# Optimization experiments

Hardware: AMD Instinct MI355X
Metric: run time of the kernel (lower is better)

The kernel has to match this reference:

```python
import jax, jax.numpy as jnp
import numpy as np

H = 8  # num_heads
EPS = 1e-5


def _lin_params(key, din, dout, scale=0.02):
    kw, _ = jax.random.split(key)
    W = jax.random.normal(kw, (din, dout), jnp.float32) * scale
    b = jnp.zeros((dout,), jnp.float32)
    return W, b


def _edge_attention(x_src, x_dst, ei, ea, Wq, bq, Wk, bk, Wv, bv, We, be, Wo, bo, n_dst):
    out_c = Wq.shape[1]
    D = out_c // H
    scale = D ** -0.5
    q = (x_dst @ Wq + bq).reshape(-1, H, D)
    k = (x_src @ Wk + bk).reshape(-1, H, D)
    v = (x_src @ Wv + bv).reshape(-1, H, D)
    e = (ea @ We + be).reshape(-1, H, D)
    src, dst = ei[0], ei[1]
    ke = k[src] + e                                # [E,H,D]
    ve = v[src] + e                                # [E,H,D]
    s = jnp.einsum('ehd,ehd->eh', q[dst], ke) * scale  # [E,H]
    # segment (per-destination) softmax, numerically stable
    m = jax.ops.segment_max(s, dst, num_segments=n_dst)
    ex = jnp.exp(s - m[dst])
    den = jax.ops.segment_sum(ex, dst, num_segments=n_dst)
    a = ex / den[dst]                              # [E,H]  (dropout = identity in eval)
    agg = jax.ops.segment_sum(a[..., None] * ve, dst, num_segments=n_dst)  # [N_dst,H,D]
    return agg.reshape(n_dst, out_c) @ Wo + bo


def _layernorm(x, g, b):
    mu = jnp.mean(x, axis=-1, keepdims=True)
    var = jnp.mean((x - mu) ** 2, axis=-1, keepdims=True)
    return (x - mu) * jax.lax.rsqrt(var + EPS) * g + b


def setup_inputs() -> dict:
    key = jax.random.key(0)
    ks = jax.random.split(key, 32)
    N_pc, N_gr, E_pp, E_pg = 50000, 8000, 400000, 100000
    din, dout, de = 128, 128, 64
    inp = {}
    inp['x_pc'] = jax.random.normal(ks[0], (N_pc, din), jnp.float32)
    inp['x_gr'] = jax.random.normal(ks[1], (N_gr, din), jnp.float32)
    inp['ea_pp'] = jax.random.normal(ks[2], (E_pp, de), jnp.float32)
    inp['ea_pg'] = jax.random.normal(ks[3], (E_pg, de), jnp.float32)
    inp['ei_pp'] = jax.random.randint(ks[4], (2, E_pp), 0, N_pc, jnp.int32)
    src_pg = jax.random.randint(ks[5], (E_pg,), 0, N_pc, jnp.int32)
    dst_pg = jax.random.randint(ks[6], (E_pg,), 0, N_gr, jnp.int32)
    inp['ei_pg'] = jnp.stack([src_pg, dst_pg])
    i = 7
    for et in ('pp', 'pg'):
        for nm, d_in in (('Wq', din), ('Wk', din), ('Wv', din), ('We', de), ('Wo', dout)):
            W, b = _lin_params(ks[i], d_in, dout); i += 1
            inp[f'{nm}_{et}'] = W
            inp[f'b{nm[1].lower()}_{et}'] = b
    for nt, d_in in (('pc', din), ('gr', din)):
        W, b = _lin_params(ks[i], d_in, dout); i += 1
        inp[f'Wnp_{nt}'] = W
        inp[f'bnp_{nt}'] = b
        inp[f'g_{nt}'] = jnp.ones((dout,), jnp.float32)
        inp[f'bln_{nt}'] = jnp.zeros((dout,), jnp.float32)
    return inp


def reference(x_pc, x_gr, ea_pp, ea_pg, ei_pp, ei_pg,
              Wq_pp, bq_pp, Wk_pp, bk_pp, Wv_pp, bv_pp, We_pp, be_pp, Wo_pp, bo_pp,
              Wq_pg, bq_pg, Wk_pg, bk_pg, Wv_pg, bv_pg, We_pg, be_pg, Wo_pg, bo_pg,
              Wnp_pc, bnp_pc, Wnp_gr, bnp_gr, g_pc, bln_pc, g_gr, bln_gr):
    N_pc, N_gr = x_pc.shape[0], x_gr.shape[0]
    out_pc = x_pc @ Wnp_pc + bnp_pc
    out_gr = x_gr @ Wnp_gr + bnp_gr
    out_pc = out_pc + _edge_attention(x_pc, x_pc, ei_pp, ea_pp,
                                      Wq_pp, bq_pp, Wk_pp, bk_pp, Wv_pp, bv_pp,
                                      We_pp, be_pp, Wo_pp, bo_pp, N_pc)
    out_gr = out_gr + _edge_attention(x_pc, x_gr, ei_pg, ea_pg,
                                      Wq_pg, bq_pg, Wk_pg, bk_pg, Wv_pg, bv_pg,
                                      We_pg, be_pg, Wo_pg, bo_pg, N_gr)
    out_pc = _layernorm(out_pc, g_pc, bln_pc)
    out_gr = _layernorm(out_gr, g_gr, bln_gr)
    return out_pc, out_gr
```

## Files before the change

kernel.cpp:

```cpp
#include <hip/hip_runtime.h>
#include <hip/hip_bf16.h>
#include <stdint.h>

typedef short short8 __attribute__((ext_vector_type(8)));
typedef float f32x4 __attribute__((ext_vector_type(4)));

__device__ __forceinline__ unsigned short f2bf(float x) {
    unsigned u = __float_as_uint(x);
    u += 0x7fffu + ((u >> 16) & 1u);
    return (unsigned short)(u >> 16);
}
__device__ __forceinline__ float bf2f(unsigned short u) {
    return __uint_as_float(((unsigned)u) << 16);
}

struct WDesc { const float* src; unsigned short* dst; int K, ldd, koff; };
struct WPack { WDesc w[12]; };

__global__ __launch_bounds__(256) void prep_weights(WPack p) {
    WDesc d = p.w[blockIdx.x];
    int total = d.K * 128;
    for (int i = threadIdx.x; i < total; i += 256) {
        int n = i / d.K, k = i - n * d.K;
        d.dst[(size_t)n * d.ldd + d.koff + k] = f2bf(d.src[(size_t)k * 128 + n]);
    }
}

struct NodeOut { const unsigned short* Wt; const float* bias; unsigned short* out; int ldc, coloff; };
struct NodePack { NodeOut d[5]; };

template <int NOUT>
__global__ __launch_bounds__(256) void gemm_node(const float* __restrict__ A, int M, NodePack dp) {
    constexpr int K = 128, LDA = 136, LDB = 72, TLD = 136;
    __shared__ __align__(16) unsigned short As[64 * LDA];
    __shared__ __align__(16) unsigned short Bs[128 * LDB];

    const int tid = threadIdx.x;
    const int rbase = blockIdx.x * 64;

    for (int slot = tid; slot < 64 * 16; slot += 256) {
        int row = slot >> 4, kg = slot & 15;
        int gr = rbase + row;
        short8 s8 = {0, 0, 0, 0, 0, 0, 0, 0};
        if (gr < M) {
            const float* a = A + (size_t)gr * K + kg * 8;
            float4 f0 = *reinterpret_cast<const float4*>(a);
            float4 f1 = *reinterpret_cast<const float4*>(a + 4);
            s8[0] = (short)f2bf(f0.x); s8[1] = (short)f2bf(f0.y);
            s8[2] = (short)f2bf(f0.z); s8[3] = (short)f2bf(f0.w);
            s8[4] = (short)f2bf(f1.x); s8[5] = (short)f2bf(f1.y);
            s8[6] = (short)f2bf(f1.z); s8[7] = (short)f2bf(f1.w);
        }
        *reinterpret_cast<short8*>(&As[row * LDA + kg * 8]) = s8;
    }

    const int lane = tid & 63, w = tid >> 6;
    const int rb = (w >> 1) * 32, cb = (w & 1) * 64;
    const int qd = lane >> 4, l16 = lane & 15;

    for (int o = 0; o < NOUT; ++o) {
        NodeOut d = dp.d[o];
        f32x4 acc[2][4];
#pragma unroll
        for (int rt = 0; rt < 2; ++rt)
#pragma unroll
            for (int ct = 0; ct < 4; ++ct) { f32x4 z = {0.f,0.f,0.f,0.f}; acc[rt][ct] = z; }

        for (int kc = 0; kc < K; kc += 64) {
            __syncthreads();
            for (int slot = tid; slot < 128 * 8; slot += 256) {
                int n = slot >> 3, kg = slot & 7;
                *reinterpret_cast<short8*>(&Bs[n * LDB + kg * 8]) =
                    *reinterpret_cast<const short8*>(d.Wt + (size_t)n * K + kc + kg * 8);
            }
            __syncthreads();
#pragma unroll
            for (int ks = 0; ks < 64; ks += 32) {
                short8 af[2], bfr[4];
#pragma unroll
                for (int rt = 0; rt < 2; ++rt)
                    af[rt] = *reinterpret_cast<const short8*>(
                        &As[(rb + rt * 16 + l16) * LDA + kc + ks + qd * 8]);
#pragma unroll
                for (int ct = 0; ct < 4; ++ct)
                    bfr[ct] = *reinterpret_cast<const short8*>(
                        &Bs[(cb + ct * 16 + l16) * LDB + ks + qd * 8]);
#pragma unroll
                for (int rt = 0; rt < 2; ++rt)
#pragma unroll
                    for (int ct = 0; ct < 4; ++ct)
                        acc[rt][ct] = __builtin_amdgcn_mfma_f32_16x16x32_bf16(
                            af[rt], bfr[ct], acc[rt][ct], 0, 0, 0);
            }
        }

        __syncthreads();
        unsigned short* tile = Bs;
#pragma unroll
        for (int ct = 0; ct < 4; ++ct) {
            int col = cb + ct * 16 + l16;
            float bv = d.bias[col];
#pragma unroll
            for (int rt = 0; rt < 2; ++rt)
#pragma unroll
                for (int r = 0; r < 4; ++r)
                    tile[(rb + rt * 16 + qd * 4 + r) * TLD + col] = f2bf(acc[rt][ct][r] + bv);
        }
        __syncthreads();
#pragma unroll
        for (int rep = 0; rep < 4; ++rep) {
            int lrow = (tid >> 4) + rep * 16, seg = tid & 15;
            int gr = rbase + lrow;
            if (gr < M)
                *reinterpret_cast<short8*>(&d.out[(size_t)gr * d.ldc + d.coloff + seg * 8]) =
                    *reinterpret_cast<const short8*>(&tile[lrow * TLD + seg * 8]);
        }
    }
}

struct EdgePack {
    const float* A; const unsigned short* Wt; const float* bias;
    const int* pos; unsigned short* out; int M;
};

__global__ __launch_bounds__(256) void gemm_edge(EdgePack p0, EdgePack p1, int B0) {
    constexpr int K = 64, LDA = 72, LDB = 72, TLD = 136;
    __shared__ __align__(16) unsigned short As[64 * LDA];
    __shared__ __align__(16) unsigned short Bs[128 * LDB];

    EdgePack p; int blk;
    if (blockIdx.x < B0) { p = p0; blk = blockIdx.x; } else { p = p1; blk = blockIdx.x - B0; }

    const int tid = threadIdx.x;
    const int rbase = blk * 64;

    for (int slot = tid; slot < 64 * 8; slot += 256) {
        int row = slot >> 3, kg = slot & 7;
        int gr = rbase + row;
        short8 s8 = {0, 0, 0, 0, 0, 0, 0, 0};
        if (gr < p.M) {
            const float* a = p.A + (size_t)gr * K + kg * 8;
            float4 f0 = *reinterpret_cast<const float4*>(a);
            float4 f1 = *reinterpret_cast<const float4*>(a + 4);
            s8[0] = (short)f2bf(f0.x); s8[1] = (short)f2bf(f0.y);
            s8[2] = (short)f2bf(f0.z); s8[3] = (short)f2bf(f0.w);
            s8[4] = (short)f2bf(f1.x); s8[5] = (short)f2bf(f1.y);
            s8[6] = (short)f2bf(f1.z); s8[7] = (short)f2bf(f1.w);
        }
        *reinterpret_cast<short8*>(&As[row * LDA + kg * 8]) = s8;
    }
    for (int slot = tid; slot < 128 * 8; slot += 256) {
        int n = slot >> 3, kg = slot & 7;
        *reinterpret_cast<short8*>(&Bs[n * LDB + kg * 8]) =
            *reinterpret_cast<const short8*>(p.Wt + (size_t)n * K + kg * 8);
    }
    __syncthreads();

    const int lane = tid & 63, w = tid >> 6;
    const int rb = (w >> 1) * 32, cb = (w & 1) * 64;
    const int qd = lane >> 4, l16 = lane & 15;

    f32x4 acc[2][4];
#pragma unroll
    for (int rt = 0; rt < 2; ++rt)
#pragma unroll
        for (int ct = 0; ct < 4; ++ct) { f32x4 z = {0.f,0.f,0.f,0.f}; acc[rt][ct] = z; }

#pragma unroll
    for (int ks = 0; ks < 64; ks += 32) {
        short8 af[2], bfr[4];
#pragma unroll
        for (int rt = 0; rt < 2; ++rt)
            af[rt] = *reinterpret_cast<const short8*>(&As[(rb + rt * 16 + l16) * LDA + ks + qd * 8]);
#pragma unroll
        for (int ct = 0; ct < 4; ++ct)
            bfr[ct] = *reinterpret_cast<const short8*>(&Bs[(cb + ct * 16 + l16) * LDB + ks + qd * 8]);
#pragma unroll
        for (int rt = 0; rt < 2; ++rt)
#pragma unroll
            for (int ct = 0; ct < 4; ++ct)
                acc[rt][ct] = __builtin_amdgcn_mfma_f32_16x16x32_bf16(
                    af[rt], bfr[ct], acc[rt][ct], 0, 0, 0);
    }

    __syncthreads();
    unsigned short* tile = Bs;
#pragma unroll
    for (int ct = 0; ct < 4; ++ct) {
        int col = cb + ct * 16 + l16;
        float bv = p.bias[col];
#pragma unroll
        for (int rt = 0; rt < 2; ++rt)
#pragma unroll
            for (int r = 0; r < 4; ++r)
                tile[(rb + rt * 16 + qd * 4 + r) * TLD + col] = f2bf(acc[rt][ct][r] + bv);
    }
    __syncthreads();
#pragma unroll
    for (int rep = 0; rep < 4; ++rep) {
        int lrow = (tid >> 4) + rep * 16, seg = tid & 15;
        int gr = rbase + lrow;
        if (gr < p.M) {
            int dp = p.pos[gr];
            *reinterpret_cast<short8*>(&p.out[(size_t)dp * 128 + seg * 8]) =
                *reinterpret_cast<const short8*>(&tile[lrow * TLD + seg * 8]);
        }
    }
}

struct OutPack {
    const unsigned short* Aagg; const float* Ax;
    const unsigned short* Wt;
    const float *bo, *bnp, *g, *bln; float* out; int M;
};

__global__ __launch_bounds__(256) void gemm_out_ln(OutPack p0, OutPack p1, int B0) {
    constexpr int K = 256, LDA = 264, LDB = 72, FTLD = 132;
    __shared__ __align__(16) char smemA[64 * LDA * 2];
    __shared__ __align__(16) unsigned short Bs[128 * LDB];
    unsigned short* As = (unsigned short*)smemA;

    OutPack p; int blk;
    if (blockIdx.x < B0) { p = p0; blk = blockIdx.x; } else { p = p1; blk = blockIdx.x - B0; }

    const int tid = threadIdx.x;
    const int rbase = blk * 64;

    for (int slot = tid; slot < 64 * 32; slot += 256) {
        int row = slot >> 5, kg = slot & 31;
        int gr = rbase + row;
        short8 s8 = {0, 0, 0, 0, 0, 0, 0, 0};
        if (gr < p.M) {
            if (kg < 16) {
                s8 = *reinterpret_cast<const short8*>(p.Aagg + (size_t)gr * 128 + kg * 8);
            } else {
                const float* a = p.Ax + (size_t)gr * 128 + (kg - 16) * 8;
                float4 f0 = *reinterpret_cast<const float4*>(a);
                float4 f1 = *reinterpret_cast<const float4*>(a + 4);
                s8[0] = (short)f2bf(f0.x); s8[1] = (short)f2bf(f0.y);
                s8[2] = (short)f2bf(f0.z); s8[3] = (short)f2bf(f0.w);
                s8[4] = (short)f2bf(f1.x); s8[5] = (short)f2bf(f1.y);
                s8[6] = (short)f2bf(f1.z); s8[7] = (short)f2bf(f1.w);
            }
        }
        *reinterpret_cast<short8*>(&As[row * LDA + kg * 8]) = s8;
    }

    const int lane = tid & 63, w = tid >> 6;
    const int rb = (w >> 1) * 32, cb = (w & 1) * 64;
    const int qd = lane >> 4, l16 = lane & 15;

    f32x4 acc[2][4];
#pragma unroll
    for (int rt = 0; rt < 2; ++rt)
#pragma unroll
        for (int ct = 0; ct < 4; ++ct) { f32x4 z = {0.f,0.f,0.f,0.f}; acc[rt][ct] = z; }

    for (int kc = 0; kc < K; kc += 64) {
        __syncthreads();
        for (int slot = tid; slot < 128 * 8; slot += 256) {
            int n = slot >> 3, kg = slot & 7;
            *reinterpret_cast<short8*>(&Bs[n * LDB + kg * 8]) =
                *reinterpret_cast<const short8*>(p.Wt + (size_t)n * K + kc + kg * 8);
        }
        __syncthreads();
#pragma unroll
        for (int ks = 0; ks < 64; ks += 32) {
            short8 af[2], bfr[4];
#pragma unroll
            for (int rt = 0; rt < 2; ++rt)
                af[rt] = *reinterpret_cast<const short8*>(
                    &As[(rb + rt * 16 + l16) * LDA + kc + ks + qd * 8]);
#pragma unroll
            for (int ct = 0; ct < 4; ++ct)
                bfr[ct] = *reinterpret_cast<const short8*>(
                    &Bs[(cb + ct * 16 + l16) * LDB + ks + qd * 8]);
#pragma unroll
            for (int rt = 0; rt < 2; ++rt)
#pragma unroll
                for (int ct = 0; ct < 4; ++ct)
                    acc[rt][ct] = __builtin_amdgcn_mfma_f32_16x16x32_bf16(
                        af[rt], bfr[ct], acc[rt][ct], 0, 0, 0);
        }
    }

    __syncthreads();
    float* ftile = (float*)smemA;
#pragma unroll
    for (int ct = 0; ct < 4; ++ct) {
        int col = cb + ct * 16 + l16;
        float bv = p.bo[col] + p.bnp[col];
#pragma unroll
        for (int rt = 0; rt < 2; ++rt)
#pragma unroll
            for (int r = 0; r < 4; ++r)
                ftile[(rb + rt * 16 + qd * 4 + r) * FTLD + col] = acc[rt][ct][r] + bv;
    }
    __syncthreads();

    int r = tid >> 2, q4 = tid & 3;
    const float* rowp = &ftile[r * FTLD + q4 * 32];
    float s = 0.f, sq = 0.f;
#pragma unroll
    for (int j = 0; j < 8; ++j) {
        float4 v = *reinterpret_cast<const float4*>(rowp + j * 4);
        s += v.x + v.y + v.z + v.w;
        sq += v.x * v.x + v.y * v.y + v.z * v.z + v.w * v.w;
    }
    s += __shfl_xor(s, 1, 64);  s += __shfl_xor(s, 2, 64);
    sq += __shfl_xor(sq, 1, 64); sq += __shfl_xor(sq, 2, 64);
    float mu = s * (1.f / 128.f);
    float var = sq * (1.f / 128.f) - mu * mu;
    float rs = rsqrtf(var + 1e-5f);
    int gr = rbase + r;
    if (gr < p.M) {
#pragma unroll
        for (int j = 0; j < 8; ++j) {
            float4 v = *reinterpret_cast<const float4*>(rowp + j * 4);
            int c = q4 * 32 + j * 4;
            float4 gg = *reinterpret_cast<const float4*>(p.g + c);
            float4 bb = *reinterpret_cast<const float4*>(p.bln + c);
            float4 o;
            o.x = (v.x - mu) * rs * gg.x + bb.x;
            o.y = (v.y - mu) * rs * gg.y + bb.y;
            o.z = (v.z - mu) * rs * gg.z + bb.z;
            o.w = (v.w - mu) * rs * gg.w + bb.w;
            *reinterpret_cast<float4*>(&p.out[(size_t)gr * 128 + c]) = o;
        }
    }
}

__global__ __launch_bounds__(256) void count_both(const int* __restrict__ d0, int E0, int* c0,
                                                  const int* __restrict__ d1, int E1, int* c1) {
    int t = blockIdx.x * 256 + threadIdx.x;
    if (t < E0) atomicAdd(&c0[d0[t]], 1);
    else if (t < E0 + E1) atomicAdd(&c1[d1[t - E0]], 1);
}

__global__ __launch_bounds__(1024) void scan_partial(const int* c0, int N0, int* rp0, int* bs0, int B0,
                                                     const int* c1, int N1, int* rp1, int* bs1) {
    __shared__ int wsum[16];
    const int* c; int* rp; int* bs; int N; int blk;
    if ((int)blockIdx.x < B0) { c = c0; rp = rp0; bs = bs0; N = N0; blk = blockIdx.x; }
    else { c = c1; rp = rp1; bs = bs1; N = N1; blk = blockIdx.x - B0; }
    int tid = threadIdx.x, lane = tid & 63, w = tid >> 6;
    int i = blk * 1024 + tid;
    int v = (i < N) ? c[i] : 0;
    int s = v;
#pragma unroll
    for (int off = 1; off < 64; off <<= 1) {
        int t = __shfl_up(s, off, 64);
        if (lane >= off) s += t;
    }
    if (lane == 63) wsum[w] = s;
    __syncthreads();
    if (w == 0 && lane < 16) {
        int ws = wsum[lane];
#pragma unroll
        for (int off = 1; off < 16; off <<= 1) {
            int t = __shfl_up(ws, off, 64);
            if (lane >= off) ws += t;
        }
        wsum[lane] = ws;
    }
    __syncthreads();
    int wexcl = (w == 0) ? 0 : wsum[w - 1];
    if (i < N) rp[i] = wexcl + s - v;
    if (tid == 0) bs[blk] = wsum[15];
}

__global__ __launch_bounds__(128) void scan_mid(const int* bs0, int* off0, int B0, int* rpN0,
                                                const int* bs1, int* off1, int B1, int* rpN1) {
    int w = threadIdx.x >> 6, lane = threadIdx.x & 63;
    const int* bs = w ? bs1 : bs0;
    int* off = w ? off1 : off0;
    int B = w ? B1 : B0;
    int* rpN = w ? rpN1 : rpN0;
    int v = (lane < B) ? bs[lane] : 0;
    int s = v;
#pragma unroll
    for (int o = 1; o < 64; o <<= 1) {
        int t = __shfl_up(s, o, 64);
        if (lane >= o) s += t;
    }
    if (lane < B) off[lane] = s - v;
    int total = __shfl(s, B - 1, 64);
    if (lane == 0) *rpN = total;
}

__global__ __launch_bounds__(1024) void scan_add(int* rp0, int* cur0, const int* off0, int N0, int B0,
                                                 int* rp1, int* cur1, const int* off1, int N1) {
    int* rp; int* cur; const int* off; int N; int blk;
    if ((int)blockIdx.x < B0) { rp = rp0; cur = cur0; off = off0; N = N0; blk = blockIdx.x; }
    else { rp = rp1; cur = cur1; off = off1; N = N1; blk = blockIdx.x - B0; }
    int i = blk * 1024 + threadIdx.x;
    if (i < N) {
        int vv = rp[i] + off[blk];
        rp[i] = vv;
        cur[i] = vv;
    }
}

__global__ __launch_bounds__(256) void scatter_both(
    const int* __restrict__ s0, const int* __restrict__ d0, int E0, int* cur0, int* pos0, int* srcs0,
    const int* __restrict__ s1, const int* __restrict__ d1, int E1, int* cur1, int* pos1, int* srcs1) {
    int t = blockIdx.x * 256 + threadIdx.x;
    if (t < E0) {
        int p = atomicAdd(&cur0[d0[t]], 1);
        pos0[t] = p;
        srcs0[p] = s0[t];
    } else if (t < E0 + E1) {
        int tt = t - E0;
        int p = atomicAdd(&cur1[d1[tt]], 1);
        pos1[tt] = p;
        srcs1[p] = s1[tt];
    }
}

struct AttnPack {
    const unsigned short *q, *kv, *e;
    const int *srcs, *row_ptr;
    unsigned short* agg; int N;
};

__global__ __launch_bounds__(256) void attn_gather(AttnPack a0, AttnPack a1, int B0) {
    AttnPack a; int blk;
    if ((int)blockIdx.x < B0) { a = a0; blk = blockIdx.x; } else { a = a1; blk = blockIdx.x - B0; }
    int wl = (blk * 256 + threadIdx.x) >> 6;
    int dst = wl >> 1;
    if (dst >= a.N) return;
    int lane = threadIdx.x & 63;
    int col = ((wl & 1) << 6) + lane;

    float qf = bf2f(a.q[(size_t)dst * 128 + col]);
    int beg = a.row_ptr[dst], end = a.row_ptr[dst + 1];
    float den = 0.f, acc = 0.f;

    float kfC = 0.f, vfC = 0.f, efC = 0.f;
    int sB = 0;
    if (beg < end) {
        int s0 = a.srcs[beg];
        kfC = bf2f(a.kv[(size_t)s0 * 256 + col]);
        vfC = bf2f(a.kv[(size_t)s0 * 256 + 128 + col]);
        efC = bf2f(a.e[(size_t)beg * 128 + col]);
        if (beg + 1 < end) sB = a.srcs[beg + 1];
    }
    for (int i = beg; i < end; ++i) {
        float kfN = 0.f, vfN = 0.f, efN = 0.f;
        int sC = 0;
        if (i + 1 < end) {
            kfN = bf2f(a.kv[(size_t)sB * 256 + col]);
            vfN = bf2f(a.kv[(size_t)sB * 256 + 128 + col]);
            efN = bf2f(a.e[(size_t)(i + 1) * 128 + col]);
            if (i + 2 < end) sC = a.srcs[i + 2];
        }
        float p = qf * (kfC + efC);
        p += __shfl_xor(p, 1, 64);
        p += __shfl_xor(p, 2, 64);
        p += __shfl_xor(p, 4, 64);
        p += __shfl_xor(p, 8, 64);
        float ex = __expf(p * 0.25f);
        den += ex;
        acc += ex * (vfC + efC);
        kfC = kfN; vfC = vfN; efC = efN; sB = sC;
    }
    a.agg[(size_t)dst * 128 + col] = f2bf(den > 0.f ? acc / den : 0.f);
}

extern "C" void kernel_launch(void* const* d_in, const int* in_sizes, int n_in,
                              void* d_out, int out_size, void* d_ws, size_t ws_size,
                              hipStream_t stream) {
    const float* x_pc  = (const float*)d_in[0];
    const float* x_gr  = (const float*)d_in[1];
    const float* ea_pp = (const float*)d_in[2];
    const float* ea_pg = (const float*)d_in[3];
    const int* ei_pp   = (const int*)d_in[4];
    const int* ei_pg   = (const int*)d_in[5];
    const float *Wq_pp = (const float*)d_in[6],  *bq_pp = (const float*)d_in[7];
    const float *Wk_pp = (const float*)d_in[8],  *bk_pp = (const float*)d_in[9];
    const float *Wv_pp = (const float*)d_in[10], *bv_pp = (const float*)d_in[11];
    const float *We_pp = (const float*)d_in[12], *be_pp = (const float*)d_in[13];
    const float *Wo_pp = (const float*)d_in[14], *bo_pp = (const float*)d_in[15];
    const float *Wq_pg = (const float*)d_in[16], *bq_pg = (const float*)d_in[17];
    const float *Wk_pg = (const float*)d_in[18], *bk_pg = (const float*)d_in[19];
    const float *Wv_pg = (const float*)d_in[20], *bv_pg = (const float*)d_in[21];
    const float *We_pg = (const float*)d_in[22], *be_pg = (const float*)d_in[23];
    const float *Wo_pg = (const float*)d_in[24], *bo_pg = (const float*)d_in[25];
    const float *Wnp_pc = (const float*)d_in[26], *bnp_pc = (const float*)d_in[27];
    const float *g_pc   = (const float*)d_in[28], *bln_pc = (const float*)d_in[29];
    const float *Wnp_gr = (const float*)d_in[30], *bnp_gr = (const float*)d_in[31];
    const float *g_gr   = (const float*)d_in[32], *bln_gr = (const float*)d_in[33];

    const int N_pc = in_sizes[0] / 128;
    const int N_gr = in_sizes[1] / 128;
    const int E_pp = in_sizes[4] / 2;
    const int E_pg = in_sizes[5] / 2;

    char* ws = (char*)d_ws;
    size_t off = 0;
    auto alloc = [&](size_t bytes) -> char* {
        char* p = ws + off;
        off += (bytes + 255) & ~(size_t)255;
        return p;
    };
    unsigned short* Wt_q_pp = (unsigned short*)alloc(128 * 128 * 2);
    unsigned short* Wt_k_pp = (unsigned short*)alloc(128 * 128 * 2);
    unsigned short* Wt_v_pp = (unsigned short*)alloc(128 * 128 * 2);
    unsigned short* Wt_k_pg = (unsigned short*)alloc(128 * 128 * 2);
    unsigned short* Wt_v_pg = (unsigned short*)alloc(128 * 128 * 2);
    unsigned short* Wt_q_pg = (unsigned short*)alloc(128 * 128 * 2);
    unsigned short* Wt_e_pp = (unsigned short*)alloc(64 * 128 * 2);
    unsigned short* Wt_e_pg = (unsigned short*)alloc(64 * 128 * 2);
    unsigned short* Wt_cat_pp = (unsigned short*)alloc(256 * 128 * 2);
    unsigned short* Wt_cat_gr = (unsigned short*)alloc(256 * 128 * 2);

    unsigned short* q_pp  = (unsigned short*)alloc((size_t)N_pc * 128 * 2);
    unsigned short* kv_pp = (unsigned short*)alloc((size_t)N_pc * 256 * 2);
    unsigned short* q_pg  = (unsigned short*)alloc((size_t)N_gr * 128 * 2);
    unsigned short* kv_pg = (unsigned short*)alloc((size_t)N_pc * 256 * 2);
    unsigned short* e_pp  = (unsigned short*)alloc((size_t)E_pp * 128 * 2);
    unsigned short* e_pg  = (unsigned short*)alloc((size_t)E_pg * 128 * 2);
    unsigned short* agg_pp = (unsigned short*)alloc((size_t)N_pc * 128 * 2);
    unsigned short* agg_pg = (unsigned short*)alloc((size_t)N_gr * 128 * 2);
    int* row_ptr_pp = (int*)alloc((size_t)(N_pc + 1) * 4);
    int* cursor_pp  = (int*)alloc((size_t)N_pc * 4);
    int* pos_pp     = (int*)alloc((size_t)E_pp * 4);
    int* srcs_pp    = (int*)alloc((size_t)E_pp * 4);
    int* row_ptr_pg = (int*)alloc((size_t)(N_gr + 1) * 4);
    int* cursor_pg  = (int*)alloc((size_t)N_gr * 4);
    int* pos_pg     = (int*)alloc((size_t)E_pg * 4);
    int* srcs_pg    = (int*)alloc((size_t)E_pg * 4);
    int* bsum_pp    = (int*)alloc(64 * 4);
    int* boff_pp    = (int*)alloc(64 * 4);
    int* bsum_pg    = (int*)alloc(64 * 4);
    int* boff_pg    = (int*)alloc(64 * 4);
    char* zbase = ws + off;
    int* counts_pp = (int*)alloc((size_t)N_pc * 4);
    int* counts_pg = (int*)alloc((size_t)N_gr * 4);
    size_t zbytes = (size_t)((ws + off) - zbase);
    hipMemsetAsync(zbase, 0, zbytes, stream);

    float* out_pc = (float*)d_out;
    float* out_gr = out_pc + (size_t)N_pc * 128;

    const int* src_pp = ei_pp;
    const int* dst_pp = ei_pp + E_pp;
    const int* src_pg = ei_pg;
    const int* dst_pg = ei_pg + E_pg;

    WPack wp;
    wp.w[0]  = {Wq_pp, Wt_q_pp, 128, 128, 0};
    wp.w[1]  = {Wk_pp, Wt_k_pp, 128, 128, 0};
    wp.w[2]  = {Wv_pp, Wt_v_pp, 128, 128, 0};
    wp.w[3]  = {Wk_pg, Wt_k_pg, 128, 128, 0};
    wp.w[4]  = {Wv_pg, Wt_v_pg, 128, 128, 0};
    wp.w[5]  = {Wq_pg, Wt_q_pg, 128, 128, 0};
    wp.w[6]  = {We_pp, Wt_e_pp, 64, 64, 0};
    wp.w[7]  = {We_pg, Wt_e_pg, 64, 64, 0};
    wp.w[8]  = {Wo_pp, Wt_cat_pp, 128, 256, 0};
    wp.w[9]  = {Wnp_pc, Wt_cat_pp, 128, 256, 128};
    wp.w[10] = {Wo_pg, Wt_cat_gr, 128, 256, 0};
    wp.w[11] = {Wnp_gr, Wt_cat_gr, 128, 256, 128};
    prep_weights<<<12, 256, 0, stream>>>(wp);

    const int Bs_pp = (N_pc + 1023) / 1024, Bs_pg = (N_gr + 1023) / 1024;
    const int gE = (E_pp + E_pg + 255) / 256;
    count_both<<<gE, 256, 0, stream>>>(dst_pp, E_pp, counts_pp, dst_pg, E_pg, counts_pg);
    scan_partial<<<Bs_pp + Bs_pg, 1024, 0, stream>>>(counts_pp, N_pc, row_ptr_pp, bsum_pp, Bs_pp,
                                                     counts_pg, N_gr, row_ptr_pg, bsum_pg);
    scan_mid<<<1, 128, 0, stream>>>(bsum_pp, boff_pp, Bs_pp, &row_ptr_pp[N_pc],
                                    bsum_pg, boff_pg, Bs_pg, &row_ptr_pg[N_gr]);
    scan_add<<<Bs_pp + Bs_pg, 1024, 0, stream>>>(row_ptr_pp, cursor_pp, boff_pp, N_pc, Bs_pp,
                                                 row_ptr_pg, cursor_pg, boff_pg, N_gr);
    scatter_both<<<gE, 256, 0, stream>>>(src_pp, dst_pp, E_pp, cursor_pp, pos_pp, srcs_pp,
                                         src_pg, dst_pg, E_pg, cursor_pg, pos_pg, srcs_pg);

    NodePack np;
    np.d[0] = {Wt_q_pp, bq_pp, q_pp, 128, 0};
    np.d[1] = {Wt_k_pp, bk_pp, kv_pp, 256, 0};
    np.d[2] = {Wt_v_pp, bv_pp, kv_pp, 256, 128};
    np.d[3] = {Wt_k_pg, bk_pg, kv_pg, 256, 0};
    np.d[4] = {Wt_v_pg, bv_pg, kv_pg, 256, 128};
    gemm_node<5><<<(N_pc + 63) / 64, 256, 0, stream>>>(x_pc, N_pc, np);
    NodePack ng{};
    ng.d[0] = {Wt_q_pg, bq_pg, q_pg, 128, 0};
    gemm_node<1><<<(N_gr + 63) / 64, 256, 0, stream>>>(x_gr, N_gr, ng);

    EdgePack ep0 = {ea_pp, Wt_e_pp, be_pp, pos_pp, e_pp, E_pp};
    EdgePack ep1 = {ea_pg, Wt_e_pg, be_pg, pos_pg, e_pg, E_pg};
    int Be0 = (E_pp + 63) / 64, Be1 = (E_pg + 63) / 64;
    gemm_edge<<<Be0 + Be1, 256, 0, stream>>>(ep0, ep1, Be0);

    AttnPack ap0 = {q_pp, kv_pp, e_pp, srcs_pp, row_ptr_pp, agg_pp, N_pc};
    AttnPack ap1 = {q_pg, kv_pg, e_pg, srcs_pg, row_ptr_pg, agg_pg, N_gr};
    int Ba0 = (N_pc + 1) / 2, Ba1 = (N_gr + 1) / 2;
    attn_gather<<<Ba0 + Ba1, 256, 0, stream>>>(ap0, ap1, Ba0);

    OutPack op0 = {agg_pp, x_pc, Wt_cat_pp, bo_pp, bnp_pc, g_pc, bln_pc, out_pc, N_pc};
    OutPack op1 = {agg_pg, x_gr, Wt_cat_gr, bo_pg, bnp_gr, g_gr, bln_gr, out_gr, N_gr};
    int Bo0 = (N_pc + 63) / 64, Bo1 = (N_gr + 63) / 64;
    gemm_out_ln<<<Bo0 + Bo1, 256, 0, stream>>>(op0, op1, Bo0);
}
```

Baseline: 564.7 us.

## Pack bf16 column pairs so one wave handles a full destination row

Intermediate q/kv/e/agg tensors are stored interleaved, with columns c and c+64 packed into one 32-bit word. Each 64-lane wave of the attention gather now processes a whole destination node with 4-byte loads instead of two waves doing 2-byte loads. The Wo weight rows are permuted to match the interleaved agg layout. Weight prep is fused with edge counting, the two node GEMMs are merged into one launch, and srcs/e are padded so the prefetch of the next edge needs no bounds check. This relies on the padded zeroed tail and on the permuted layout being consistent everywhere it is read.

```diff
diff --git a/kernel.cpp b/kernel.cpp
--- a/kernel.cpp
+++ b/kernel.cpp
@@ -10,33 +10,48 @@
     u += 0x7fffu + ((u >> 16) & 1u);
     return (unsigned short)(u >> 16);
 }
-__device__ __forceinline__ float bf2f(unsigned short u) {
-    return __uint_as_float(((unsigned)u) << 16);
-}
-
-struct WDesc { const float* src; unsigned short* dst; int K, ldd, koff; };
+__device__ __forceinline__ float bflo(unsigned u) { return __uint_as_float(u << 16); }
+__device__ __forceinline__ float bfhi(unsigned u) { return __uint_as_float(u & 0xffff0000u); }
+
+struct WDesc { const float* src; unsigned short* dst; int K, ldd, koff, perm; };
 struct WPack { WDesc w[12]; };
 
-__global__ __launch_bounds__(256) void prep_weights(WPack p) {
-    WDesc d = p.w[blockIdx.x];
-    int total = d.K * 128;
-    for (int i = threadIdx.x; i < total; i += 256) {
-        int n = i / d.K, k = i - n * d.K;
-        d.dst[(size_t)n * d.ldd + d.koff + k] = f2bf(d.src[(size_t)k * 128 + n]);
-    }
-}
-
-struct NodeOut { const unsigned short* Wt; const float* bias; unsigned short* out; int ldc, coloff; };
-struct NodePack { NodeOut d[5]; };
-
-template <int NOUT>
-__global__ __launch_bounds__(256) void gemm_node(const float* __restrict__ A, int M, NodePack dp) {
-    constexpr int K = 128, LDA = 136, LDB = 72, TLD = 136;
+__global__ __launch_bounds__(256) void prep_and_count(WPack p,
+        const int* __restrict__ d0, int E0, int* c0,
+        const int* __restrict__ d1, int E1, int* c1, int nPrep) {
+    if ((int)blockIdx.x < nPrep) {
+        int wi = blockIdx.x >> 2, chunk = blockIdx.x & 3;
+        WDesc d = p.w[wi];
+        int total = d.K * 128, cs = total >> 2;
+        int lo = chunk * cs, hi = lo + cs;
+        for (int i = lo + threadIdx.x; i < hi; i += 256) {
+            int n = i / d.K, k = i - n * d.K;
+            int kk = d.perm ? (2 * (k & 63) + (k >> 6)) : k;
+            d.dst[(size_t)n * d.ldd + d.koff + kk] = f2bf(d.src[(size_t)k * 128 + n]);
+        }
+    } else {
+        int t = (blockIdx.x - nPrep) * 256 + threadIdx.x;
+        if (t < E0) atomicAdd(&c0[d0[t]], 1);
+        else if (t < E0 + E1) atomicAdd(&c1[d1[t - E0]], 1);
+    }
+}
+
+struct NodeOut { const unsigned short* Wt; const float* bias; unsigned int* out; int ldc, coloff; };
+struct NodePack { NodeOut d[5]; int nout; };
+
+__global__ __launch_bounds__(256) void gemm_node(const float* __restrict__ A0, int M0, NodePack p0,
+                                                 int B0,
+                                                 const float* __restrict__ A1, int M1, NodePack p1) {
+    constexpr int K = 128, LDA = 136, LDB = 72, TLD = 133;
     __shared__ __align__(16) unsigned short As[64 * LDA];
     __shared__ __align__(16) unsigned short Bs[128 * LDB];
 
+    const float* A; int M; NodePack dp; int blk;
+    if ((int)blockIdx.x < B0) { A = A0; M = M0; dp = p0; blk = blockIdx.x; }
+    else { A = A1; M = M1; dp = p1; blk = blockIdx.x - B0; }
+
     const int tid = threadIdx.x;
-    const int rbase = blockIdx.x * 64;
+    const int rbase = blk * 64;
 
     for (int slot = tid; slot < 64 * 16; slot += 256) {
         int row = slot >> 4, kg = slot & 15;
@@ -58,7 +73,7 @@
     const int rb = (w >> 1) * 32, cb = (w & 1) * 64;
     const int qd = lane >> 4, l16 = lane & 15;
 
-    for (int o = 0; o < NOUT; ++o) {
+    for (int o = 0; o < dp.nout; ++o) {
         NodeOut d = dp.d[o];
         f32x4 acc[2][4];
 #pragma unroll
@@ -111,25 +126,33 @@
         for (int rep = 0; rep < 4; ++rep) {
             int lrow = (tid >> 4) + rep * 16, seg = tid & 15;
             int gr = rbase + lrow;
-            if (gr < M)
-                *reinterpret_cast<short8*>(&d.out[(size_t)gr * d.ldc + d.coloff + seg * 8]) =
-                    *reinterpret_cast<const short8*>(&tile[lrow * TLD + seg * 8]);
+            if (gr < M) {
+                uint4 pk;
+#pragma unroll
+                for (int j = 0; j < 4; ++j) {
+                    int pcol = seg * 4 + j;
+                    unsigned lo16 = tile[lrow * TLD + pcol];
+                    unsigned hi16 = tile[lrow * TLD + pcol + 64];
+                    ((unsigned*)&pk)[j] = lo16 | (hi16 << 16);
+                }
+                *reinterpret_cast<uint4*>(&d.out[(size_t)gr * d.ldc + d.coloff + seg * 4]) = pk;
+            }
         }
     }
 }
 
 struct EdgePack {
     const float* A; const unsigned short* Wt; const float* bias;
-    const int* pos; unsigned short* out; int M;
+    const int* pos; unsigned int* out; int M;
 };
 
 __global__ __launch_bounds__(256) void gemm_edge(EdgePack p0, EdgePack p1, int B0) {
-    constexpr int K = 64, LDA = 72, LDB = 72, TLD = 136;
+    constexpr int K = 64, LDA = 72, LDB = 72, TLD = 133;
     __shared__ __align__(16) unsigned short As[64 * LDA];
     __shared__ __align__(16) unsigned short Bs[128 * LDB];
 
     EdgePack p; int blk;
-    if (blockIdx.x < B0) { p = p0; blk = blockIdx.x; } else { p = p1; blk = blockIdx.x - B0; }
+    if ((int)blockIdx.x < B0) { p = p0; blk = blockIdx.x; } else { p = p1; blk = blockIdx.x - B0; }
 
     const int tid = threadIdx.x;
     const int rbase = blk * 64;
@@ -201,9 +224,16 @@
         int lrow = (tid >> 4) + rep * 16, seg = tid & 15;
         int gr = rbase + lrow;
         if (gr < p.M) {
-            int dp = p.pos[gr];
-            *reinterpret_cast<short8*>(&p.out[(size_t)dp * 128 + seg * 8]) =
-                *reinterpret_cast<const short8*>(&tile[lrow * TLD + seg * 8]);
+            int dpos = p.pos[gr];
+            uint4 pk;
+#pragma unroll
+            for (int j = 0; j < 4; ++j) {
+                int pcol = seg * 4 + j;
+                unsigned lo16 = tile[lrow * TLD + pcol];
+                unsigned hi16 = tile[lrow * TLD + pcol + 64];
+                ((unsigned*)&pk)[j] = lo16 | (hi16 << 16);
+            }
+            *reinterpret_cast<uint4*>(&p.out[(size_t)dpos * 64 + seg * 4]) = pk;
         }
     }
 }
@@ -221,7 +251,7 @@
     unsigned short* As = (unsigned short*)smemA;
 
     OutPack p; int blk;
-    if (blockIdx.x < B0) { p = p0; blk = blockIdx.x; } else { p = p1; blk = blockIdx.x - B0; }
+    if ((int)blockIdx.x < B0) { p = p0; blk = blockIdx.x; } else { p = p1; blk = blockIdx.x - B0; }
 
     const int tid = threadIdx.x;
     const int rbase = blk * 64;
@@ -330,13 +360,6 @@
     }
 }
 
-__global__ __launch_bounds__(256) void count_both(const int* __restrict__ d0, int E0, int* c0,
-                                                  const int* __restrict__ d1, int E1, int* c1) {
-    int t = blockIdx.x * 256 + threadIdx.x;
-    if (t < E0) atomicAdd(&c0[d0[t]], 1);
-    else if (t < E0 + E1) atomicAdd(&c1[d1[t - E0]], 1);
-}
-
 __global__ __launch_bounds__(1024) void scan_partial(const int* c0, int N0, int* rp0, int* bs0, int B0,
                                                      const int* c1, int N1, int* rp1, int* bs1) {
     __shared__ int wsum[16];
@@ -418,53 +441,53 @@
 }
 
 struct AttnPack {
-    const unsigned short *q, *kv, *e;
-    const int *srcs, *row_ptr;
-    unsigned short* agg; int N;
+    const unsigned int *q, *kv, *e;
+    const int *srcs;
+    const int *row_ptr;
+    unsigned int* agg; int N;
 };
 
 __global__ __launch_bounds__(256) void attn_gather(AttnPack a0, AttnPack a1, int B0) {
     AttnPack a; int blk;
     if ((int)blockIdx.x < B0) { a = a0; blk = blockIdx.x; } else { a = a1; blk = blockIdx.x - B0; }
-    int wl = (blk * 256 + threadIdx.x) >> 6;
-    int dst = wl >> 1;
+    int dst = blk * 4 + (threadIdx.x >> 6);
     if (dst >= a.N) return;
     int lane = threadIdx.x & 63;
-    int col = ((wl & 1) << 6) + lane;
-
-    float qf = bf2f(a.q[(size_t)dst * 128 + col]);
+
+    unsigned qp = a.q[(size_t)dst * 64 + lane];
+    float qlo = bflo(qp), qhi = bfhi(qp);
     int beg = a.row_ptr[dst], end = a.row_ptr[dst + 1];
-    float den = 0.f, acc = 0.f;
-
-    float kfC = 0.f, vfC = 0.f, efC = 0.f;
-    int sB = 0;
-    if (beg < end) {
-        int s0 = a.srcs[beg];
-        kfC = bf2f(a.kv[(size_t)s0 * 256 + col]);
-        vfC = bf2f(a.kv[(size_t)s0 * 256 + 128 + col]);
-        efC = bf2f(a.e[(size_t)beg * 128 + col]);
-        if (beg + 1 < end) sB = a.srcs[beg + 1];
-    }
+    float denl = 0.f, denh = 0.f, accl = 0.f, acch = 0.f;
+
+    int sC = a.srcs[beg];
+    unsigned kC = a.kv[(size_t)sC * 128 + lane];
+    unsigned vC = a.kv[(size_t)sC * 128 + 64 + lane];
+    unsigned eC = a.e[(size_t)beg * 64 + lane];
+
     for (int i = beg; i < end; ++i) {
-        float kfN = 0.f, vfN = 0.f, efN = 0.f;
-        int sC = 0;
-        if (i + 1 < end) {
-            kfN = bf2f(a.kv[(size_t)sB * 256 + col]);
-            vfN = bf2f(a.kv[(size_t)sB * 256 + 128 + col]);
-            efN = bf2f(a.e[(size_t)(i + 1) * 128 + col]);
-            if (i + 2 < end) sC = a.srcs[i + 2];
-        }
-        float p = qf * (kfC + efC);
-        p += __shfl_xor(p, 1, 64);
-        p += __shfl_xor(p, 2, 64);
-        p += __shfl_xor(p, 4, 64);
-        p += __shfl_xor(p, 8, 64);
-        float ex = __expf(p * 0.25f);
-        den += ex;
-        acc += ex * (vfC + efC);
-        kfC = kfN; vfC = vfN; efC = efN; sB = sC;
-    }
-    a.agg[(size_t)dst * 128 + col] = f2bf(den > 0.f ? acc / den : 0.f);
+        int sN = a.srcs[i + 1];
+        unsigned kN = a.kv[(size_t)sN * 128 + lane];
+        unsigned vN = a.kv[(size_t)sN * 128 + 64 + lane];
+        unsigned eN = a.e[(size_t)(i + 1) * 64 + lane];
+
+        float kl = bflo(kC), kh = bfhi(kC);
+        float vl = bflo(vC), vh = bfhi(vC);
+        float el = bflo(eC), eh = bfhi(eC);
+        float pl = qlo * (kl + el), ph = qhi * (kh + eh);
+#pragma unroll
+        for (int m = 1; m < 16; m <<= 1) {
+            pl += __shfl_xor(pl, m, 64);
+            ph += __shfl_xor(ph, m, 64);
+        }
+        float exl = __expf(pl * 0.25f), exh = __expf(ph * 0.25f);
+        denl += exl; denh += exh;
+        accl += exl * (vl + el);
+        acch += exh * (vh + eh);
+        kC = kN; vC = vN; eC = eN;
+    }
+    float ol = denl > 0.f ? accl / denl : 0.f;
+    float oh = denh > 0.f ? acch / denh : 0.f;
+    a.agg[(size_t)dst * 64 + lane] = (unsigned)f2bf(ol) | ((unsigned)f2bf(oh) << 16);
 }
 
 extern "C" void kernel_launch(void* const* d_in, const int* in_sizes, int n_in,
@@ -514,22 +537,20 @@
     unsigned short* Wt_cat_pp = (unsigned short*)alloc(256 * 128 * 2);
     unsigned short* Wt_cat_gr = (unsigned short*)alloc(256 * 128 * 2);
 
-    unsigned short* q_pp  = (unsigned short*)alloc((size_t)N_pc * 128 * 2);
-    unsigned short* kv_pp = (unsigned short*)alloc((size_t)N_pc * 256 * 2);
-    unsigned short* q_pg  = (unsigned short*)alloc((size_t)N_gr * 128 * 2);
-    unsigned short* kv_pg = (unsigned short*)alloc((size_t)N_pc * 256 * 2);
-    unsigned short* e_pp  = (unsigned short*)alloc((size_t)E_pp * 128 * 2);
-    unsigned short* e_pg  = (unsigned short*)alloc((size_t)E_pg * 128 * 2);
-    unsigned short* agg_pp = (unsigned short*)alloc((size_t)N_pc * 128 * 2);
-    unsigned short* agg_pg = (unsigned short*)alloc((size_t)N_gr * 128 * 2);
+    unsigned int* q_pp  = (unsigned int*)alloc((size_t)N_pc * 64 * 4);
+    unsigned int* kv_pp = (unsigned int*)alloc((size_t)N_pc * 128 * 4);
+    unsigned int* q_pg  = (unsigned int*)alloc((size_t)N_gr * 64 * 4);
+    unsigned int* kv_pg = (unsigned int*)alloc((size_t)N_pc * 128 * 4);
+    unsigned int* e_pp  = (unsigned int*)alloc((size_t)(E_pp + 1) * 64 * 4);
+    unsigned int* e_pg  = (unsigned int*)alloc((size_t)(E_pg + 1) * 64 * 4);
+    unsigned int* agg_pp = (unsigned int*)alloc((size_t)N_pc * 64 * 4);
+    unsigned int* agg_pg = (unsigned int*)alloc((size_t)N_gr * 64 * 4);
     int* row_ptr_pp = (int*)alloc((size_t)(N_pc + 1) * 4);
     int* cursor_pp  = (int*)alloc((size_t)N_pc * 4);
     int* pos_pp     = (int*)alloc((size_t)E_pp * 4);
-    int* srcs_pp    = (int*)alloc((size_t)E_pp * 4);
     int* row_ptr_pg = (int*)alloc((size_t)(N_gr + 1) * 4);
     int* cursor_pg  = (int*)alloc((size_t)N_gr * 4);
     int* pos_pg     = (int*)alloc((size_t)E_pg * 4);
-    int* srcs_pg    = (int*)alloc((size_t)E_pg * 4);
     int* bsum_pp    = (int*)alloc(64 * 4);
     int* boff_pp    = (int*)alloc(64 * 4);
     int* bsum_pg    = (int*)alloc(64 * 4);
@@ -537,6 +558,8 @@
     char* zbase = ws + off;
     int* counts_pp = (int*)alloc((size_t)N_pc * 4);
     int* counts_pg = (int*)alloc((size_t)N_gr * 4);
+    int* srcs_pp   = (int*)alloc((size_t)(E_pp + 8) * 4);
+    int* srcs_pg   = (int*)alloc((size_t)(E_pg + 8) * 4);
     size_t zbytes = (size_t)((ws + off) - zbase);
     hipMemsetAsync(zbase, 0, zbytes, stream);
 
@@ -549,23 +572,24 @@
     const int* dst_pg = ei_pg + E_pg;
 
     WPack wp;
-    wp.w[0]  = {Wq_pp, Wt_q_pp, 128, 128, 0};
-    wp.w[1]  = {Wk_pp, Wt_k_pp, 128, 128, 0};
-    wp.w[2]  = {Wv_pp, Wt_v_pp, 128, 128, 0};
-    wp.w[3]  = {Wk_pg, Wt_k_pg, 128, 128, 0};
-    wp.w[4]  = {Wv_pg, Wt_v_pg, 128, 128, 0};
-    wp.w[5]  = {Wq_pg, Wt_q_pg, 128, 128, 0};
-    wp.w[6]  = {We_pp, Wt_e_pp, 64, 64, 0};
-    wp.w[7]  = {We_pg, Wt_e_pg, 64, 64, 0};
-    wp.w[8]  = {Wo_pp, Wt_cat_pp, 128, 256, 0};
-    wp.w[9]  = {Wnp_pc, Wt_cat_pp, 128, 256, 128};
-    wp.w[10] = {Wo_pg, Wt_cat_gr, 128, 256, 0};
-    wp.w[11] = {Wnp_gr, Wt_cat_gr, 128, 256, 128};
-    prep_weights<<<12, 256, 0, stream>>>(wp);
+    wp.w[0]  = {Wq_pp, Wt_q_pp, 128, 128, 0, 0};
+    wp.w[1]  = {Wk_pp, Wt_k_pp, 128, 128, 0, 0};
+    wp.w[2]  = {Wv_pp, Wt_v_pp, 128, 128, 0, 0};
+    wp.w[3]  = {Wk_pg, Wt_k_pg, 128, 128, 0, 0};
+    wp.w[4]  = {Wv_pg, Wt_v_pg, 128, 128, 0, 0};
+    wp.w[5]  = {Wq_pg, Wt_q_pg, 128, 128, 0, 0};
+    wp.w[6]  = {We_pp, Wt_e_pp, 64, 64, 0, 0};
+    wp.w[7]  = {We_pg, Wt_e_pg, 64, 64, 0, 0};
+    wp.w[8]  = {Wo_pp, Wt_cat_pp, 128, 256, 0, 1};
+    wp.w[9]  = {Wnp_pc, Wt_cat_pp, 128, 256, 128, 0};
+    wp.w[10] = {Wo_pg, Wt_cat_gr, 128, 256, 0, 1};
+    wp.w[11] = {Wnp_gr, Wt_cat_gr, 128, 256, 128, 0};
+    const int NPREP = 48;
+    const int gE = (E_pp + E_pg + 255) / 256;
+    prep_and_count<<<NPREP + gE, 256, 0, stream>>>(wp, dst_pp, E_pp, counts_pp,
+                                                   dst_pg, E_pg, counts_pg, NPREP);
 
     const int Bs_pp = (N_pc + 1023) / 1024, Bs_pg = (N_gr + 1023) / 1024;
-    const int gE = (E_pp + E_pg + 255) / 256;
-    count_both<<<gE, 256, 0, stream>>>(dst_pp, E_pp, counts_pp, dst_pg, E_pg, counts_pg);
     scan_partial<<<Bs_pp + Bs_pg, 1024, 0, stream>>>(counts_pp, N_pc, row_ptr_pp, bsum_pp, Bs_pp,
                                                      counts_pg, N_gr, row_ptr_pg, bsum_pg);
     scan_mid<<<1, 128, 0, stream>>>(bsum_pp, boff_pp, Bs_pp, &row_ptr_pp[N_pc],
@@ -576,15 +600,17 @@
                                          src_pg, dst_pg, E_pg, cursor_pg, pos_pg, srcs_pg);
 
     NodePack np;
-    np.d[0] = {Wt_q_pp, bq_pp, q_pp, 128, 0};
-    np.d[1] = {Wt_k_pp, bk_pp, kv_pp, 256, 0};
-    np.d[2] = {Wt_v_pp, bv_pp, kv_pp, 256, 128};
-    np.d[3] = {Wt_k_pg, bk_pg, kv_pg, 256, 0};
-    np.d[4] = {Wt_v_pg, bv_pg, kv_pg, 256, 128};
-    gemm_node<5><<<(N_pc + 63) / 64, 256, 0, stream>>>(x_pc, N_pc, np);
+    np.d[0] = {Wt_q_pp, bq_pp, q_pp, 64, 0};
+    np.d[1] = {Wt_k_pp, bk_pp, kv_pp, 128, 0};
+    np.d[2] = {Wt_v_pp, bv_pp, kv_pp, 128, 64};
+    np.d[3] = {Wt_k_pg, bk_pg, kv_pg, 128, 0};
+    np.d[4] = {Wt_v_pg, bv_pg, kv_pg, 128, 64};
+    np.nout = 5;
     NodePack ng{};
-    ng.d[0] = {Wt_q_pg, bq_pg, q_pg, 128, 0};
-    gemm_node<1><<<(N_gr + 63) / 64, 256, 0, stream>>>(x_gr, N_gr, ng);
+    ng.d[0] = {Wt_q_pg, bq_pg, q_pg, 64, 0};
+    ng.nout = 1;
+    int Bn0 = (N_pc + 63) / 64, Bn1 = (N_gr + 63) / 64;
+    gemm_node<<<Bn0 + Bn1, 256, 0, stream>>>(x_pc, N_pc, np, Bn0, x_gr, N_gr, ng);
 
     EdgePack ep0 = {ea_pp, Wt_e_pp, be_pp, pos_pp, e_pp, E_pp};
     EdgePack ep1 = {ea_pg, Wt_e_pg, be_pg, pos_pg, e_pg, E_pg};
@@ -593,11 +619,11 @@
 
     AttnPack ap0 = {q_pp, kv_pp, e_pp, srcs_pp, row_ptr_pp, agg_pp, N_pc};
     AttnPack ap1 = {q_pg, kv_pg, e_pg, srcs_pg, row_ptr_pg, agg_pg, N_gr};
-    int Ba0 = (N_pc + 1) / 2, Ba1 = (N_gr + 1) / 2;
+    int Ba0 = (N_pc + 3) / 4, Ba1 = (N_gr + 3) / 4;
     attn_gather<<<Ba0 + Ba1, 256, 0, stream>>>(ap0, ap1, Ba0);
 
-    OutPack op0 = {agg_pp, x_pc, Wt_cat_pp, bo_pp, bnp_pc, g_pc, bln_pc, out_pc, N_pc};
-    OutPack op1 = {agg_pg, x_gr, Wt_cat_gr, bo_pg, bnp_gr, g_gr, bln_gr, out_gr, N_gr};
+    OutPack op0 = {(const unsigned short*)agg_pp, x_pc, Wt_cat_pp, bo_pp, bnp_pc, g_pc, bln_pc, out_pc, N_pc};
+    OutPack op1 = {(const unsigned short*)agg_pg, x_gr, Wt_cat_gr, bo_pg, bnp_gr, g_gr, bln_gr, out_gr, N_gr};
     int Bo0 = (N_pc + 63) / 64, Bo1 = (N_gr + 63) / 64;
     gemm_out_ln<<<Bo0 + Bo1, 256, 0, stream>>>(op0, op1, Bo0);
 }
```

Result: faster. 532.8 us (-5.6%).
